# Optimization experiments

Measured on AMD Instinct MI355X. Metric: run time of the kernel, lower is better.

The kernel has to match this reference:

```python
import jax, jax.numpy as jnp
import numpy as np
from jax import lax

N = 5000
C = 81  # num_classes including background at index 0
BG_OFFSET = 1


def _iou_matrix(b):
    # b: [N,4] as x1,y1,x2,y2 -> pairwise IoU [N,N]
    x1, y1, x2, y2 = b[:, 0], b[:, 1], b[:, 2], b[:, 3]
    area = (x2 - x1) * (y2 - y1)  # [N]
    ix1 = jnp.maximum(x1[:, None], x1[None, :])
    iy1 = jnp.maximum(y1[:, None], y1[None, :])
    ix2 = jnp.minimum(x2[:, None], x2[None, :])
    iy2 = jnp.minimum(y2[:, None], y2[None, :])
    iw = jnp.maximum(ix2 - ix1, 0.0)
    ih = jnp.maximum(iy2 - iy1, 0.0)
    inter = iw * ih
    return inter / (area[:, None] + area[None, :] - inter)


def setup_inputs() -> dict:
    key = jax.random.key(0)
    k1, k2, k3 = jax.random.split(key, 3)
    # valid boxes: x1<x2, y1<y2 on a ~1024px canvas, size ~up to 256px
    xy1 = jax.random.uniform(k1, (N, 2), dtype=jnp.float32) * 1024.0
    wh = jax.random.uniform(k2, (N, 2), dtype=jnp.float32) * 256.0 + 1.0
    bboxes = jnp.concatenate([xy1, xy1 + wh], axis=1)  # [N,4]
    scores = jax.random.uniform(k3, (N, C), dtype=jnp.float32)  # [N,C]
    return {
        "bboxes": bboxes,
        "scores": scores,
        "conf_thresh": 0.6,
        "nms_thresh": 0.5,
        "max_instances": 300,
    }


def _multiclass_nms(bboxes, scores, conf_thresh, nms_thresh, max_instances):
    n = bboxes.shape[0]
    neg_inf = jnp.finfo(scores.dtype).min
    iou = _iou_matrix(bboxes)  # [N,N]

    def nms_one_class(score_c):  # score_c: [N]
        valid = score_c > conf_thresh
        masked = jnp.where(valid, score_c, neg_inf)
        order = jnp.argsort(masked)[::-1]  # descending score

        def step(suppressed, idx):
            keep = valid[idx] & ~suppressed[idx]
            new_sup = jnp.where(keep, suppressed | (iou[idx] > nms_thresh), suppressed)
            return new_sup, keep

        _, keeps = lax.scan(step, jnp.zeros((n,), bool), order)
        # scatter keep flags back to original box order
        return jnp.zeros((n,), bool).at[order].set(keeps)

    fg_scores = scores[:, BG_OFFSET:].T  # [C-1, N]
    keep = jax.vmap(nms_one_class)(fg_scores)  # [C-1, N]

    # global top-k over all (class, box) kept detections, sorted by score desc
    flat = jnp.where(keep, fg_scores, neg_inf).reshape(-1)  # [(C-1)*N]
    top_scores, top_idx = lax.top_k(flat, max_instances)
    cls = top_idx // n + BG_OFFSET  # [K]
    box = top_idx % n  # [K]
    valid_out = top_scores > neg_inf / 2

    sel_score = scores[box, cls]  # differentiable gather
    preds = jnp.concatenate([bboxes[box], sel_score[:, None]], axis=1)  # [K,5]
    preds = jnp.where(valid_out[:, None], preds, 0.0)
    labels = jnp.where(valid_out, cls, -1)
    return preds, labels


def reference(bboxes, scores, conf_thresh, nms_thresh, max_instances):
    return _multiclass_nms(bboxes, scores, conf_thresh, nms_thresh, max_instances)
```

## Files before the change

kernel.cpp:

```cpp
#include <hip/hip_runtime.h>

typedef unsigned long long u64;
typedef unsigned int u32;
typedef unsigned short u16;

#define MSORT 4096
#define TPB1  1024
#define TPBF  1024
#define BOXCAP 3648
#define KCAP  3072
#define RSLOT_W 10
#define KPC   300
#define SELCAP 1024
#define PREFR 64

#define WG_SCOPE  __HIP_MEMORY_SCOPE_WORKGROUP
#define DEV_SCOPE __HIP_MEMORY_SCOPE_AGENT

__device__ __forceinline__ float boxArea(float4 b) {
    return __fmul_rn(__fsub_rn(b.z, b.x), __fsub_rn(b.w, b.y));
}

template<bool GE>
__device__ __forceinline__ bool iou_gt(float4 a, float area_a, float4 b, float area_b, double B) {
    float ix1 = fmaxf(a.x, b.x), iy1 = fmaxf(a.y, b.y);
    float ix2 = fminf(a.z, b.z), iy2 = fminf(a.w, b.w);
    float iw  = fmaxf(__fsub_rn(ix2, ix1), 0.0f);
    float ih  = fmaxf(__fsub_rn(iy2, iy1), 0.0f);
    float inter = __fmul_rn(iw, ih);
    float uni   = __fsub_rn(__fadd_rn(area_a, area_b), inter);
    return GE ? ((double)inter >= B * (double)uni) : ((double)inter > B * (double)uni);
}

__device__ __forceinline__ int scoreBin(u32 bits) {
    int b = (int)(bits >> 12) - 0x3F000;
    return b < 0 ? 0 : (b > 2047 ? 2047 : b);
}

__device__ __forceinline__ void bstar_wave0(
    const u32* __restrict__ hist, int target, int tid,
    int* __restrict__ outBs, int* __restrict__ outTot)
{
    if (tid < 64) {
        int s = 0;
        #pragma unroll
        for (int b = 0; b < 32; b++)
            s += (int)hist[(tid << 5) + ((b + tid) & 31)];
        #pragma unroll
        for (int d = 1; d < 64; d <<= 1) {
            int v = __shfl_down(s, d, 64);
            if (tid + d < 64) s += v;
        }
        u64 bal = __ballot(s >= target);
        int ch  = bal ? (63 - __builtin_clzll(bal)) : -1;
        int tot = __shfl(s, 0, 64);
        int bs  = 0;
        if (ch >= 0) {
            int accAbove = (ch < 63) ? __shfl(s, ch + 1, 64) : 0;
            int h = (tid < 32) ? (int)hist[(ch << 5) + tid] : 0;
            #pragma unroll
            for (int d = 1; d < 32; d <<= 1) {
                int v = __shfl_down(h, d, 64);
                if (tid + d < 32) h += v;
            }
            u64 bal2 = __ballot((tid < 32) && (accAbove + h >= target));
            bs = (ch << 5) + (63 - __builtin_clzll(bal2));
        }
        if (tid == 0) { *outBs = bs; if (outTot) *outTot = tot; }
    }
}

template<bool GE>
__device__ __forceinline__ int prefix_nms_w0(
    const float* __restrict__ bboxes, const u64* __restrict__ sorted,
    int R, double B, int tid, int c, int N, u64* __restrict__ gkept_c,
    u32* __restrict__ gHist)
{
    u64 key = (tid < R) ? sorted[tid] : 0;
    float4 bx = make_float4(0.f, 0.f, 0.f, 0.f);
    if (tid < R) bx = ((const float4*)bboxes)[(u32)key];
    float ar = boxArea(bx);
    u64 supB = (R >= 64) ? 0ull : (~0ull << R);
    int nk = 0;
    int i = -1;
    for (;;) {
        u64 mask = (i >= 63) ? 0ull : (~0ull << (i + 1));
        u64 alive = ~supB & mask;
        if (!alive) break;
        i = (int)__builtin_ctzll(alive);
        float4 bi;
        bi.x = __shfl(bx.x, i, 64); bi.y = __shfl(bx.y, i, 64);
        bi.z = __shfl(bx.z, i, 64); bi.w = __shfl(bx.w, i, 64);
        float ai = boxArea(bi);
        if (tid == 0) {
            u64 ki = sorted[i];
            u32 flat = (u32)c * (u32)N + (u32)ki;
            gkept_c[nk] = (ki & 0xFFFFFFFF00000000ull) | (u32)(~flat);
        }
        nk++;
        bool sup = (tid > i) && iou_gt<GE>(bi, ai, bx, ar, B);
        supB |= __ballot(sup);
    }
    if (tid < R && !((supB >> tid) & 1ull))
        atomicAdd(&gHist[scoreBin((u32)(key >> 32))], 1u);
    return nk;
}

__global__ __launch_bounds__(TPB1, 1) void nms_select_kernel(
    const float* __restrict__ bboxes, const float* __restrict__ scores,
    const float* __restrict__ conf_ptr, const float* __restrict__ nms_ptr,
    int N, int C, u64* __restrict__ gkept,
    u32* __restrict__ gK, u32* __restrict__ g65, u32* __restrict__ gPre,
    u32* __restrict__ gHist, u32* __restrict__ gCtl, u32* __restrict__ gDone,
    int Mout)
{
    __shared__ u64 keys[KCAP];
    __shared__ u32 hist[2048];
    __shared__ u64 keybuf[256];
    __shared__ u64 sorted[66];
    __shared__ int cntS, ncollS, bstarS, nkS, lastS, thBs, thTot;

    const int tid = threadIdx.x;
    const int c   = blockIdx.x;
    const int cls = c + 1;
    const float conf = *conf_ptr;
    const float nmsT = *nms_ptr;

    for (int b = tid; b < 2048; b += TPB1) hist[b] = 0;
    if (tid < 66) sorted[tid] = 0;
    if (tid == 0) { cntS = 0; ncollS = 0; nkS = 0; }
    __syncthreads();

    for (int i = tid; i < N; i += TPB1) {
        float s = scores[(size_t)i * C + cls];
        if (s > conf) {
            int p = atomicAdd(&cntS, 1);
            if (p < KCAP) keys[p] = ((u64)__float_as_uint(s) << 32) | (u32)i;
            atomicAdd(&hist[scoreBin(__float_as_uint(s))], 1u);
        }
    }
    __syncthreads();
    const int K = cntS;
    const bool preOv = (K > KCAP);
    const int target = K < (PREFR + 1) ? K : (PREFR + 1);

    bstar_wave0(hist, target, tid, &bstarS, nullptr);
    __syncthreads();
    const u32 tbits = (bstarS == 0) ? 0u : (((u32)bstarS + 0x3F000u) << 12);

    const int KL = K < KCAP ? K : KCAP;
    for (int p = tid; p < KL; p += TPB1) {
        u64 k = keys[p];
        if ((u32)(k >> 32) >= tbits) {
            int pos = atomicAdd(&ncollS, 1);
            if (pos < 256) keybuf[pos] = k;
        }
    }
    __syncthreads();
    const int ncoll = ncollS;
    const bool pre = preOv || (ncoll > 256);
    for (int p = ncoll + tid; p < 256; p += TPB1) keybuf[p] = 0;
    __syncthreads();

    u64* gkept_c = gkept + (size_t)c * KPC;
    if (!pre) {
        if (tid < 256) {
            u64 my = keybuf[tid];
            int rank = 0;
            for (int j = 0; j < 256; j++) rank += (keybuf[j] > my);
            if (my && rank < PREFR + 1) sorted[rank] = my;
        }
        __syncthreads();
        const u32 tb = __float_as_uint(nmsT);
        const float Tn = __uint_as_float(tb + 1u);
        const double B = ((double)nmsT + (double)Tn) * 0.5;
        const bool geCmp = (((tb + 1u) & 1u) == 0u);
        if (tid < 64) {
            int R = ncoll < PREFR ? ncoll : PREFR;
            int nk = geCmp ? prefix_nms_w0<true >(bboxes, sorted, R, B, tid, c, N, gkept_c, gHist)
                           : prefix_nms_w0<false>(bboxes, sorted, R, B, tid, c, N, gkept_c, gHist);
            if (tid == 0) nkS = nk;
        }
        __syncthreads();
        for (int p = nkS + tid; p < KPC; p += TPB1) gkept_c[p] = 0;
    } else {
        for (int p = tid; p < KPC; p += TPB1) gkept_c[p] = 0;
    }
    if (tid == 0) {
        gK[c]   = (u32)K;
        g65[c]  = pre ? 0xFFFFFFFFu : ((ncoll >= PREFR + 1) ? (u32)(sorted[PREFR] >> 32) : 0u);
        gPre[c] = pre ? 1u : 0u;
    }

    __syncthreads();
    if (tid == 0)
        lastS = (__hip_atomic_fetch_add(gDone, 1u, __ATOMIC_ACQ_REL, DEV_SCOPE)
                 == (u32)(gridDim.x - 1)) ? 1 : 0;
    __syncthreads();
    if (!lastS) return;
    __threadfence();

    for (int b = tid; b < 2048; b += TPB1) hist[b] = gHist[b];
    __syncthreads();
    bstar_wave0(hist, Mout, tid, &thBs, &thTot);
    __syncthreads();
    u32 theta = 0u;
    if (thTot >= Mout && thBs > 0) theta = (((u32)thBs + 0x3F000u) << 12);
    if (tid == 0) gCtl[0] = theta;
    const int nclass = (int)gridDim.x;
    for (int c2 = tid; c2 < nclass; c2 += TPB1) {
        u32 need = gPre[c2];
        if (gK[c2] > PREFR && g65[c2] >= theta) need = 1u;
        gCtl[1 + c2] = need;
    }
}

template<bool GE>
__device__ __forceinline__ u64 sweep_own(
    float4 bi, float area_i, const float4 (&breg)[RSLOT_W],
    const float (&areaj)[RSLOT_W], const float4* __restrict__ boxesLds,
    int base, int nslots, int lane, double B)
{
    u64 ns = 0;
    #pragma unroll
    for (int t = 0; t < RSLOT_W; t++)
        ns |= ((u64)iou_gt<GE>(bi, area_i, breg[t], areaj[t], B)) << (base + t);
    for (int t = RSLOT_W; t < nslots; t++) {
        float4 bj = boxesLds[((base + t) << 6) | lane];
        ns |= ((u64)iou_gt<GE>(bi, area_i, bj, boxArea(bj), B)) << (base + t);
    }
    return ns;
}

template<bool GE>
__device__ __forceinline__ int greedy_full(
    const float4* __restrict__ boxesLds, u16* __restrict__ keptR,
    float4* __restrict__ pubBox, u32* __restrict__ ctl,
    const u32* __restrict__ gsi_c, const float* __restrict__ scores,
    int cls, int C, u32 thetaBits,
    int K, int smax, double B, int lane, int wave)
{
    const int SW   = (smax + 3) >> 2;
    const int base = (wave * SW < smax) ? wave * SW : smax;
    const int end  = (base + SW < smax) ? base + SW : smax;
    const int nslots = end - base;

    float4 breg[RSLOT_W];
    float  areaj[RSLOT_W];
    #pragma unroll
    for (int t = 0; t < RSLOT_W; t++) {
        float4 b = boxesLds[((base + t) << 6) | lane];
        breg[t] = b;
        areaj[t] = boxArea(b);
    }

    u64 sup;
    {
        int t = (lane < K) ? ((K - lane + 63) >> 6) : 0;
        sup = (t >= 64) ? 0ull : (~0ull << t);
    }

    u32 seen = 0;
    if (wave != 0) {
        for (;;) {
            u32 d  = __hip_atomic_load(&ctl[2], __ATOMIC_ACQUIRE, WG_SCOPE);
            u32 cn = __hip_atomic_load(&ctl[0], __ATOMIC_ACQUIRE, WG_SCOPE);
            bool prog = (seen < cn);
            while (seen < cn) {
                float4 bi = pubBox[seen]; seen++;
                sup |= sweep_own<GE>(bi, boxArea(bi), breg, areaj, boxesLds, base, nslots, lane, B);
            }
            if (d) return -1;
            u32 aw = __hip_atomic_load(&ctl[1], __ATOMIC_ACQUIRE, WG_SCOPE);
            if (aw == (u32)wave) {
                u32 cn2 = __hip_atomic_load(&ctl[0], __ATOMIC_ACQUIRE, WG_SCOPE);
                while (seen < cn2) {
                    float4 bi = pubBox[seen]; seen++;
                    sup |= sweep_own<GE>(bi, boxArea(bi), breg, areaj, boxesLds, base, nslots, lane, B);
                }
                break;
            }
            if (!prog) __builtin_amdgcn_s_sleep(1);
        }
    }

    u32 nk = seen;
    const u32 seen0 = seen;
    int scur = base - 1;
    float4 bcur = make_float4(0.f, 0.f, 0.f, 0.f);
    float  acur = 0.f;
    int js = base << 6;

    for (;;) {
        int s = js >> 6;
        while (s > scur) {
            scur++;
            if (scur < end) {
                bcur = boxesLds[(scur << 6) | lane];
                acur = boxArea(bcur);
                u64 bit = 0;
                for (u32 k = seen0; k < nk; k++) {
                    float4 bk = pubBox[k];
                    bit |= ((u64)iou_gt<GE>(bk, boxArea(bk), bcur, acur, B));
                }
                sup |= bit << scur;
            }
        }
        if (scur >= end) {
            if (wave == 3) {
                if (lane == 0) __hip_atomic_store(&ctl[2], 1u, __ATOMIC_RELEASE, WG_SCOPE);
                return (int)nk;
            }
            if (lane == 0) __hip_atomic_store(&ctl[1], (u32)(wave + 1), __ATOMIC_RELEASE, WG_SCOPE);
            return -1;
        }
        u64 bal = __ballot((int)(((~sup) >> scur) & 1ull)) & (~0ull << (js & 63));
        if (bal == 0) { js = (scur + 1) << 6; continue; }
        int i = (scur << 6) + (int)__builtin_ctzll(bal);

        if (thetaBits) {
            u32 idx = gsi_c[i];
            float sc = scores[(size_t)idx * C + cls];
            if (__float_as_uint(sc) < thetaBits) {
                if (lane == 0) __hip_atomic_store(&ctl[2], 1u, __ATOMIC_RELEASE, WG_SCOPE);
                return (int)nk;
            }
        }
        float4 bi = boxesLds[i];
        if (lane == 0) { pubBox[nk] = bi; keptR[nk] = (u16)i; }
        nk++;
        if (nk >= KPC) {
            if (lane == 0) {
                __hip_atomic_store(&ctl[0], nk, __ATOMIC_RELEASE, WG_SCOPE);
                __hip_atomic_store(&ctl[2], 1u, __ATOMIC_RELEASE, WG_SCOPE);
            }
            return (int)nk;
        }
        if (lane == 0) __hip_atomic_store(&ctl[0], nk, __ATOMIC_RELEASE, WG_SCOPE);
        sup |= ((u64)iou_gt<GE>(bi, boxArea(bi), bcur, acur, B)) << scur;
        js = i + 1;
    }
}

__global__ __launch_bounds__(TPBF, 1) void nms_full_topk_kernel(
    const float* __restrict__ bboxes, const float* __restrict__ scores,
    const float* __restrict__ conf_ptr, const float* __restrict__ nms_ptr,
    int N, int C, const u32* __restrict__ gCtl,
    u32* __restrict__ gsi, u64* __restrict__ gkept,
    int Mout, float* __restrict__ out, u32* __restrict__ gDone)
{
    __shared__ __align__(16) char smem[63856];
    __shared__ int cntS, lastS, selCountS, bs4S;

    const int c = blockIdx.x;
    const int tid = threadIdx.x;

    if (gCtl[1 + c] != 0u) {
        u64*    sortbuf  = (u64*)smem;
        float4* boxesLds = (float4*)smem;
        u16*    keptR    = (u16*)(smem + 58368);
        u32*    ctl      = (u32*)(smem + 58976);
        float4* pubBox   = (float4*)(smem + 58992);

        const int cls = c + 1;
        const float conf = *conf_ptr;
        const float nmsT = *nms_ptr;
        const u32 thetaBits = gCtl[0];

        if (tid == 0) cntS = 0;
        __syncthreads();
        for (int i = tid; i < N; i += TPBF) {
            float s = scores[(size_t)i * C + cls];
            if (s > conf) {
                int p = atomicAdd(&cntS, 1);
                if (p < MSORT) sortbuf[p] = ((u64)__float_as_uint(s) << 32) | (u32)i;
            }
        }
        __syncthreads();
        int K = cntS; if (K > BOXCAP) K = BOXCAP;
        int M = 64; while (M < K) M <<= 1;
        for (int p = K + tid; p < M; p += TPBF) sortbuf[p] = 0;
        __syncthreads();
        for (int kk = 2; kk <= M; kk <<= 1) {
            for (int j = kk >> 1; j > 0; j >>= 1) {
                for (int i = tid; i < M; i += TPBF) {
                    int ixj = i ^ j;
                    if (ixj > i) {
                        u64 a = sortbuf[i], b = sortbuf[ixj];
                        if (((i & kk) == 0) ? (a < b) : (a > b)) { sortbuf[i] = b; sortbuf[ixj] = a; }
                    }
                }
                __syncthreads();
            }
        }
        u32 myIdx[MSORT / TPBF];
        #pragma unroll
        for (int t = 0; t < MSORT / TPBF; t++) myIdx[t] = (u32)sortbuf[t * TPBF + tid];
        __syncthreads();
        u32* gsi_c = gsi + (size_t)c * BOXCAP;
        #pragma unroll
        for (int t = 0; t < MSORT / TPBF; t++) {
            int r = t * TPBF + tid;
            if (r < K) {
                u32 idx = myIdx[t];
                gsi_c[r] = idx;
                boxesLds[r] = ((const float4*)bboxes)[idx];
            }
        }
        if (tid == 0) { ctl[0] = 0; ctl[1] = 0; ctl[2] = 0; }
        __syncthreads();

        if (tid < 256) {
            const int lane = tid & 63;
            const int wave = tid >> 6;
            const u32 tb = __float_as_uint(nmsT);
            const float Tn = __uint_as_float(tb + 1u);
            const double B = ((double)nmsT + (double)Tn) * 0.5;
            const bool geCmp = (((tb + 1u) & 1u) == 0u);
            const int smax = (K + 63) >> 6;

            int ret = geCmp ? greedy_full<true >(boxesLds, keptR, pubBox, ctl, gsi_c, scores, cls, C, thetaBits, K, smax, B, lane, wave)
                            : greedy_full<false>(boxesLds, keptR, pubBox, ctl, gsi_c, scores, cls, C, thetaBits, K, smax, B, lane, wave);
            if (ret >= 0) {
                int kept = ret; if (kept > KPC) kept = KPC;
                u64* gkept_c = gkept + (size_t)c * KPC;
                for (int p = lane; p < kept; p += 64) {
                    int rank = keptR[p];
                    u32 idx = gsi_c[rank];
                    float sc = scores[(size_t)idx * C + cls];
                    u32 flat = (u32)c * (u32)N + idx;
                    gkept_c[p] = ((u64)__float_as_uint(sc) << 32) | (u32)(~flat);
                }
                for (int p = kept + lane; p < KPC; p += 64) gkept_c[p] = 0;
            }
        }
    }

    __syncthreads();
    if (tid == 0)
        lastS = (__hip_atomic_fetch_add(gDone, 1u, __ATOMIC_ACQ_REL, DEV_SCOPE)
                 == (u32)(gridDim.x - 1)) ? 1 : 0;
    __syncthreads();
    if (!lastS) return;
    __threadfence();

    u64* sel   = (u64*)smem;
    u32* hist4 = (u32*)(smem + 8192);
    const int total = (int)gridDim.x * KPC;

    for (int b = tid; b < 2048; b += TPBF) hist4[b] = 0;
    if (tid == 0) selCountS = 0;
    __syncthreads();

    for (int t = tid; t < total; t += TPBF) {
        u64 k = gkept[t];
        if (k) atomicAdd(&hist4[scoreBin((u32)(k >> 32))], 1u);
    }
    __syncthreads();

    bstar_wave0(hist4, Mout, tid, &bs4S, nullptr);
    __syncthreads();
    const int bstar = bs4S;

    for (int t = tid; t < total; t += TPBF) {
        u64 k = gkept[t];
        if (k && scoreBin((u32)(k >> 32)) >= bstar) {
            int p = atomicAdd(&selCountS, 1);
            if (p < SELCAP) sel[p] = k;
        }
    }
    __syncthreads();
    int cnt = selCountS; if (cnt > SELCAP) cnt = SELCAP;
    int SM = 512; while (SM < cnt) SM <<= 1;
    for (int p = cnt + tid; p < SM; p += TPBF) sel[p] = 0;
    __syncthreads();

    for (int kk = 2; kk <= SM; kk <<= 1) {
        for (int j = kk >> 1; j > 0; j >>= 1) {
            for (int i = tid; i < SM; i += TPBF) {
                int ixj = i ^ j;
                if (ixj > i) {
                    u64 a = sel[i], b = sel[ixj];
                    if (((i & kk) == 0) ? (a < b) : (a > b)) { sel[i] = b; sel[ixj] = a; }
                }
            }
            __syncthreads();
        }
    }

    for (int t = tid; t < Mout; t += TPBF) {
        u64 k = (t < SM) ? sel[t] : 0;
        float px1 = 0.f, py1 = 0.f, px2 = 0.f, py2 = 0.f, ps = 0.f, plab = -1.0f;
        if (k) {
            float s  = __uint_as_float((u32)(k >> 32));
            u32 flat = ~((u32)k);
            int cc   = (int)(flat / (u32)N);
            int box  = (int)(flat - (u32)cc * (u32)N);
            float4 bb = ((const float4*)bboxes)[box];
            px1 = bb.x; py1 = bb.y; px2 = bb.z; py2 = bb.w; ps = s;
            plab = (float)(cc + 1);
        }
        out[t * 5 + 0] = px1;
        out[t * 5 + 1] = py1;
        out[t * 5 + 2] = px2;
        out[t * 5 + 3] = py2;
        out[t * 5 + 4] = ps;
        out[Mout * 5 + t] = plab;
    }
}

extern "C" void kernel_launch(void* const* d_in, const int* in_sizes, int n_in,
                              void* d_out, int out_size, void* d_ws, size_t ws_size,
                              hipStream_t stream) {
    const float* bboxes = (const float*)d_in[0];
    const float* scores = (const float*)d_in[1];
    const float* conf   = (const float*)d_in[2];
    const float* nmsT   = (const float*)d_in[3];

    const int N    = in_sizes[0] / 4;
    const int C    = in_sizes[1] / N;
    const int nc   = C - 1;
    const int Mout = out_size / 6;

    char* wsb = (char*)d_ws;
    size_t off = 0;
    u32* gsi   = (u32*)(wsb + off); off += (size_t)nc * BOXCAP * sizeof(u32);
    u64* gkept = (u64*)(wsb + off); off += (size_t)nc * KPC * sizeof(u64);
    u32* gK    = (u32*)(wsb + off); off += (size_t)((nc + 1) & ~1) * sizeof(u32);
    u32* g65   = (u32*)(wsb + off); off += (size_t)((nc + 1) & ~1) * sizeof(u32);
    u32* gPre  = (u32*)(wsb + off); off += (size_t)((nc + 1) & ~1) * sizeof(u32);
    u32* gCtl  = (u32*)(wsb + off); off += (size_t)((1 + nc + 1) & ~1) * sizeof(u32);
    u32* gHist = (u32*)(wsb + off); off += 2048 * sizeof(u32);
    u32* gDone = (u32*)(wsb + off); off += 2 * sizeof(u32);

    hipMemsetAsync(gHist, 0, (2048 + 2) * sizeof(u32), stream);

    nms_select_kernel<<<nc, TPB1, 0, stream>>>(bboxes, scores, conf, nmsT, N, C,
                                               gkept, gK, g65, gPre, gHist, gCtl,
                                               gDone, Mout);
    nms_full_topk_kernel<<<nc, TPBF, 0, stream>>>(bboxes, scores, conf, nmsT, N, C,
                                                  gCtl, gsi, gkept, Mout,
                                                  (float*)d_out, gDone + 1);
}
```

Baseline: 134.4 us.

## Transpose scores upfront and split last-block reductions into separate kernels

Adds a tiled transpose kernel that writes scores in class-major order, so the per-class scans read contiguous float4 rows instead of strided columns. It also replaces per-element LDS atomics with wave-aggregated ballot atomics. The last-block-done atomic pattern is replaced by standalone theta and top-k kernels, which removes the memset and device-scope atomics. The cost is an extra pass over the score matrix and three more kernel launches.

```diff
diff --git a/kernel.cpp b/kernel.cpp
--- a/kernel.cpp
+++ b/kernel.cpp
@@ -13,9 +13,9 @@
 #define KPC   300
 #define SELCAP 1024
 #define PREFR 64
-
-#define WG_SCOPE  __HIP_MEMORY_SCOPE_WORKGROUP
-#define DEV_SCOPE __HIP_MEMORY_SCOPE_AGENT
+#define TBOX  128
+
+#define WG_SCOPE __HIP_MEMORY_SCOPE_WORKGROUP
 
 __device__ __forceinline__ float boxArea(float4 b) {
     return __fmul_rn(__fsub_rn(b.z, b.x), __fsub_rn(b.w, b.y));
@@ -68,6 +68,35 @@
         }
         if (tid == 0) { *outBs = bs; if (outTot) *outTot = tot; }
     }
+}
+
+__global__ __launch_bounds__(1024) void transpose_kernel(
+    const float* __restrict__ scores, int N, int C,
+    float* __restrict__ scoresT, u32* __restrict__ gHist)
+{
+    __shared__ float tile[TBOX * 81];
+    const int tid = threadIdx.x;
+    const int b0  = blockIdx.x * TBOX;
+    const int nb  = (N - b0 < TBOX) ? (N - b0) : TBOX;
+    const int tot = nb * C;
+    for (int e = tid; e < tot; e += 1024)
+        tile[e] = scores[(size_t)b0 * C + e];
+    __syncthreads();
+    if (nb == TBOX) {
+        const int wtot = C << 7;
+        for (int o = tid; o < wtot; o += 1024) {
+            int cls = o >> 7, j = o & (TBOX - 1);
+            scoresT[(size_t)cls * N + b0 + j] = tile[j * C + cls];
+        }
+    } else {
+        const int wtot = C * nb;
+        for (int o = tid; o < wtot; o += 1024) {
+            int cls = o / nb, j = o - cls * nb;
+            scoresT[(size_t)cls * N + b0 + j] = tile[j * C + cls];
+        }
+    }
+    if (blockIdx.x == 0)
+        for (int h = tid; h < 2048; h += 1024) gHist[h] = 0;
 }
 
 template<bool GE>
@@ -107,22 +136,22 @@
 }
 
 __global__ __launch_bounds__(TPB1, 1) void nms_select_kernel(
-    const float* __restrict__ bboxes, const float* __restrict__ scores,
+    const float* __restrict__ bboxes, const float* __restrict__ scoresT,
     const float* __restrict__ conf_ptr, const float* __restrict__ nms_ptr,
-    int N, int C, u64* __restrict__ gkept,
+    int N, u64* __restrict__ gkept,
     u32* __restrict__ gK, u32* __restrict__ g65, u32* __restrict__ gPre,
-    u32* __restrict__ gHist, u32* __restrict__ gCtl, u32* __restrict__ gDone,
-    int Mout)
+    u32* __restrict__ gHist)
 {
     __shared__ u64 keys[KCAP];
     __shared__ u32 hist[2048];
     __shared__ u64 keybuf[256];
     __shared__ u64 sorted[66];
-    __shared__ int cntS, ncollS, bstarS, nkS, lastS, thBs, thTot;
-
-    const int tid = threadIdx.x;
-    const int c   = blockIdx.x;
-    const int cls = c + 1;
+    __shared__ int cntS, ncollS, bstarS, nkS;
+
+    const int tid  = threadIdx.x;
+    const int lane = tid & 63;
+    const int c    = blockIdx.x;
+    const int cls  = c + 1;
     const float conf = *conf_ptr;
     const float nmsT = *nms_ptr;
 
@@ -131,8 +160,32 @@
     if (tid == 0) { cntS = 0; ncollS = 0; nkS = 0; }
     __syncthreads();
 
-    for (int i = tid; i < N; i += TPB1) {
-        float s = scores[(size_t)i * C + cls];
+    const float* rowT = scoresT + (size_t)cls * N;
+    const float4* rowT4 = (const float4*)rowT;
+    const int N4 = N >> 2;
+    for (int i4 = tid; i4 < N4; i4 += TPB1) {
+        float4 s4 = rowT4[i4];
+        #pragma unroll
+        for (int j = 0; j < 4; j++) {
+            float s = (j == 0) ? s4.x : (j == 1) ? s4.y : (j == 2) ? s4.z : s4.w;
+            bool pass = (s > conf);
+            u64 m = __ballot(pass);
+            if (m) {
+                int leader = (int)__builtin_ctzll(m);
+                int base = 0;
+                if (lane == leader) base = atomicAdd(&cntS, __popcll(m));
+                base = __shfl(base, leader, 64);
+                if (pass) {
+                    int p = base + (int)__popcll(m & ((1ull << lane) - 1ull));
+                    if (p < KCAP)
+                        keys[p] = ((u64)__float_as_uint(s) << 32) | (u32)((i4 << 2) + j);
+                    atomicAdd(&hist[scoreBin(__float_as_uint(s))], 1u);
+                }
+            }
+        }
+    }
+    for (int i = (N4 << 2) + tid; i < N; i += TPB1) {
+        float s = rowT[i];
         if (s > conf) {
             int p = atomicAdd(&cntS, 1);
             if (p < KCAP) keys[p] = ((u64)__float_as_uint(s) << 32) | (u32)i;
@@ -191,24 +244,24 @@
         g65[c]  = pre ? 0xFFFFFFFFu : ((ncoll >= PREFR + 1) ? (u32)(sorted[PREFR] >> 32) : 0u);
         gPre[c] = pre ? 1u : 0u;
     }
-
-    __syncthreads();
-    if (tid == 0)
-        lastS = (__hip_atomic_fetch_add(gDone, 1u, __ATOMIC_ACQ_REL, DEV_SCOPE)
-                 == (u32)(gridDim.x - 1)) ? 1 : 0;
-    __syncthreads();
-    if (!lastS) return;
-    __threadfence();
-
-    for (int b = tid; b < 2048; b += TPB1) hist[b] = gHist[b];
+}
+
+__global__ __launch_bounds__(1024) void nms_theta_kernel(
+    const u32* __restrict__ gHist, const u32* __restrict__ gK,
+    const u32* __restrict__ g65, const u32* __restrict__ gPre,
+    int nc, int Mout, u32* __restrict__ gCtl)
+{
+    __shared__ u32 hist[2048];
+    __shared__ int thBs, thTot;
+    const int tid = threadIdx.x;
+    for (int b = tid; b < 2048; b += 1024) hist[b] = gHist[b];
     __syncthreads();
     bstar_wave0(hist, Mout, tid, &thBs, &thTot);
     __syncthreads();
     u32 theta = 0u;
     if (thTot >= Mout && thBs > 0) theta = (((u32)thBs + 0x3F000u) << 12);
     if (tid == 0) gCtl[0] = theta;
-    const int nclass = (int)gridDim.x;
-    for (int c2 = tid; c2 < nclass; c2 += TPB1) {
+    for (int c2 = tid; c2 < nc; c2 += 1024) {
         u32 need = gPre[c2];
         if (gK[c2] > PREFR && g65[c2] >= theta) need = 1u;
         gCtl[1 + c2] = need;
@@ -236,8 +289,8 @@
 __device__ __forceinline__ int greedy_full(
     const float4* __restrict__ boxesLds, u16* __restrict__ keptR,
     float4* __restrict__ pubBox, u32* __restrict__ ctl,
-    const u32* __restrict__ gsi_c, const float* __restrict__ scores,
-    int cls, int C, u32 thetaBits,
+    const u32* __restrict__ gsi_c, const float* __restrict__ rowT,
+    u32 thetaBits,
     int K, int smax, double B, int lane, int wave)
 {
     const int SW   = (smax + 3) >> 2;
@@ -320,7 +373,7 @@
 
         if (thetaBits) {
             u32 idx = gsi_c[i];
-            float sc = scores[(size_t)idx * C + cls];
+            float sc = rowT[idx];
             if (__float_as_uint(sc) < thetaBits) {
                 if (lane == 0) __hip_atomic_store(&ctl[2], 1u, __ATOMIC_RELEASE, WG_SCOPE);
                 return (int)nk;
@@ -342,142 +395,162 @@
     }
 }
 
-__global__ __launch_bounds__(TPBF, 1) void nms_full_topk_kernel(
-    const float* __restrict__ bboxes, const float* __restrict__ scores,
+__global__ __launch_bounds__(TPBF, 1) void nms_full_kernel(
+    const float* __restrict__ bboxes, const float* __restrict__ scoresT,
     const float* __restrict__ conf_ptr, const float* __restrict__ nms_ptr,
-    int N, int C, const u32* __restrict__ gCtl,
-    u32* __restrict__ gsi, u64* __restrict__ gkept,
-    int Mout, float* __restrict__ out, u32* __restrict__ gDone)
-{
+    int N, const u32* __restrict__ gCtl,
+    u32* __restrict__ gsi, u64* __restrict__ gkept)
+{
+    const int c = blockIdx.x;
+    if (gCtl[1 + c] == 0u) return;
+
     __shared__ __align__(16) char smem[63856];
-    __shared__ int cntS, lastS, selCountS, bs4S;
-
-    const int c = blockIdx.x;
+    u64*    sortbuf  = (u64*)smem;
+    float4* boxesLds = (float4*)smem;
+    u16*    keptR    = (u16*)(smem + 58368);
+    u32*    ctl      = (u32*)(smem + 58976);
+    float4* pubBox   = (float4*)(smem + 58992);
+    __shared__ int cntS;
+
+    const int tid  = threadIdx.x;
+    const int lane = tid & 63;
+    const int cls = c + 1;
+    const float conf = *conf_ptr;
+    const float nmsT = *nms_ptr;
+    const u32 thetaBits = gCtl[0];
+
+    if (tid == 0) cntS = 0;
+    __syncthreads();
+    const float* rowT = scoresT + (size_t)cls * N;
+    const float4* rowT4 = (const float4*)rowT;
+    const int N4 = N >> 2;
+    for (int i4 = tid; i4 < N4; i4 += TPBF) {
+        float4 s4 = rowT4[i4];
+        #pragma unroll
+        for (int j = 0; j < 4; j++) {
+            float s = (j == 0) ? s4.x : (j == 1) ? s4.y : (j == 2) ? s4.z : s4.w;
+            bool pass = (s > conf);
+            u64 m = __ballot(pass);
+            if (m) {
+                int leader = (int)__builtin_ctzll(m);
+                int base = 0;
+                if (lane == leader) base = atomicAdd(&cntS, __popcll(m));
+                base = __shfl(base, leader, 64);
+                if (pass) {
+                    int p = base + (int)__popcll(m & ((1ull << lane) - 1ull));
+                    if (p < MSORT)
+                        sortbuf[p] = ((u64)__float_as_uint(s) << 32) | (u32)((i4 << 2) + j);
+                }
+            }
+        }
+    }
+    for (int i = (N4 << 2) + tid; i < N; i += TPBF) {
+        float s = rowT[i];
+        if (s > conf) {
+            int p = atomicAdd(&cntS, 1);
+            if (p < MSORT) sortbuf[p] = ((u64)__float_as_uint(s) << 32) | (u32)i;
+        }
+    }
+    __syncthreads();
+    int K = cntS; if (K > BOXCAP) K = BOXCAP;
+    int M = 64; while (M < K) M <<= 1;
+    for (int p = K + tid; p < M; p += TPBF) sortbuf[p] = 0;
+    __syncthreads();
+    for (int kk = 2; kk <= M; kk <<= 1) {
+        for (int j = kk >> 1; j > 0; j >>= 1) {
+            for (int i = tid; i < M; i += TPBF) {
+                int ixj = i ^ j;
+                if (ixj > i) {
+                    u64 a = sortbuf[i], b = sortbuf[ixj];
+                    if (((i & kk) == 0) ? (a < b) : (a > b)) { sortbuf[i] = b; sortbuf[ixj] = a; }
+                }
+            }
+            __syncthreads();
+        }
+    }
+    u32 myIdx[MSORT / TPBF];
+    #pragma unroll
+    for (int t = 0; t < MSORT / TPBF; t++) myIdx[t] = (u32)sortbuf[t * TPBF + tid];
+    __syncthreads();
+    u32* gsi_c = gsi + (size_t)c * BOXCAP;
+    #pragma unroll
+    for (int t = 0; t < MSORT / TPBF; t++) {
+        int r = t * TPBF + tid;
+        if (r < K) {
+            u32 idx = myIdx[t];
+            gsi_c[r] = idx;
+            boxesLds[r] = ((const float4*)bboxes)[idx];
+        }
+    }
+    if (tid == 0) { ctl[0] = 0; ctl[1] = 0; ctl[2] = 0; }
+    __syncthreads();
+    if (tid >= 256) return;
+
+    const int wave = tid >> 6;
+    const u32 tb = __float_as_uint(nmsT);
+    const float Tn = __uint_as_float(tb + 1u);
+    const double B = ((double)nmsT + (double)Tn) * 0.5;
+    const bool geCmp = (((tb + 1u) & 1u) == 0u);
+    const int smax = (K + 63) >> 6;
+
+    int ret = geCmp ? greedy_full<true >(boxesLds, keptR, pubBox, ctl, gsi_c, rowT, thetaBits, K, smax, B, lane, wave)
+                    : greedy_full<false>(boxesLds, keptR, pubBox, ctl, gsi_c, rowT, thetaBits, K, smax, B, lane, wave);
+    if (ret >= 0) {
+        int kept = ret; if (kept > KPC) kept = KPC;
+        u64* gkept_c = gkept + (size_t)c * KPC;
+        for (int p = lane; p < kept; p += 64) {
+            int rank = keptR[p];
+            u32 idx = gsi_c[rank];
+            float sc = rowT[idx];
+            u32 flat = (u32)c * (u32)N + idx;
+            gkept_c[p] = ((u64)__float_as_uint(sc) << 32) | (u32)(~flat);
+        }
+        for (int p = kept + lane; p < KPC; p += 64) gkept_c[p] = 0;
+    }
+}
+
+__global__ __launch_bounds__(1024) void nms_topk_kernel(
+    const float* __restrict__ bboxes, const u64* __restrict__ gkept,
+    int N, int nc, int Mout, float* __restrict__ out)
+{
+    __shared__ u32 hist[2048];
+    __shared__ int selCount;
+    __shared__ int bstarS;
+    __shared__ u64 sel[SELCAP];
+
     const int tid = threadIdx.x;
-
-    if (gCtl[1 + c] != 0u) {
-        u64*    sortbuf  = (u64*)smem;
-        float4* boxesLds = (float4*)smem;
-        u16*    keptR    = (u16*)(smem + 58368);
-        u32*    ctl      = (u32*)(smem + 58976);
-        float4* pubBox   = (float4*)(smem + 58992);
-
-        const int cls = c + 1;
-        const float conf = *conf_ptr;
-        const float nmsT = *nms_ptr;
-        const u32 thetaBits = gCtl[0];
-
-        if (tid == 0) cntS = 0;
-        __syncthreads();
-        for (int i = tid; i < N; i += TPBF) {
-            float s = scores[(size_t)i * C + cls];
-            if (s > conf) {
-                int p = atomicAdd(&cntS, 1);
-                if (p < MSORT) sortbuf[p] = ((u64)__float_as_uint(s) << 32) | (u32)i;
-            }
-        }
-        __syncthreads();
-        int K = cntS; if (K > BOXCAP) K = BOXCAP;
-        int M = 64; while (M < K) M <<= 1;
-        for (int p = K + tid; p < M; p += TPBF) sortbuf[p] = 0;
-        __syncthreads();
-        for (int kk = 2; kk <= M; kk <<= 1) {
-            for (int j = kk >> 1; j > 0; j >>= 1) {
-                for (int i = tid; i < M; i += TPBF) {
-                    int ixj = i ^ j;
-                    if (ixj > i) {
-                        u64 a = sortbuf[i], b = sortbuf[ixj];
-                        if (((i & kk) == 0) ? (a < b) : (a > b)) { sortbuf[i] = b; sortbuf[ixj] = a; }
-                    }
-                }
-                __syncthreads();
-            }
-        }
-        u32 myIdx[MSORT / TPBF];
-        #pragma unroll
-        for (int t = 0; t < MSORT / TPBF; t++) myIdx[t] = (u32)sortbuf[t * TPBF + tid];
-        __syncthreads();
-        u32* gsi_c = gsi + (size_t)c * BOXCAP;
-        #pragma unroll
-        for (int t = 0; t < MSORT / TPBF; t++) {
-            int r = t * TPBF + tid;
-            if (r < K) {
-                u32 idx = myIdx[t];
-                gsi_c[r] = idx;
-                boxesLds[r] = ((const float4*)bboxes)[idx];
-            }
-        }
-        if (tid == 0) { ctl[0] = 0; ctl[1] = 0; ctl[2] = 0; }
-        __syncthreads();
-
-        if (tid < 256) {
-            const int lane = tid & 63;
-            const int wave = tid >> 6;
-            const u32 tb = __float_as_uint(nmsT);
-            const float Tn = __uint_as_float(tb + 1u);
-            const double B = ((double)nmsT + (double)Tn) * 0.5;
-            const bool geCmp = (((tb + 1u) & 1u) == 0u);
-            const int smax = (K + 63) >> 6;
-
-            int ret = geCmp ? greedy_full<true >(boxesLds, keptR, pubBox, ctl, gsi_c, scores, cls, C, thetaBits, K, smax, B, lane, wave)
-                            : greedy_full<false>(boxesLds, keptR, pubBox, ctl, gsi_c, scores, cls, C, thetaBits, K, smax, B, lane, wave);
-            if (ret >= 0) {
-                int kept = ret; if (kept > KPC) kept = KPC;
-                u64* gkept_c = gkept + (size_t)c * KPC;
-                for (int p = lane; p < kept; p += 64) {
-                    int rank = keptR[p];
-                    u32 idx = gsi_c[rank];
-                    float sc = scores[(size_t)idx * C + cls];
-                    u32 flat = (u32)c * (u32)N + idx;
-                    gkept_c[p] = ((u64)__float_as_uint(sc) << 32) | (u32)(~flat);
-                }
-                for (int p = kept + lane; p < KPC; p += 64) gkept_c[p] = 0;
-            }
-        }
-    }
-
-    __syncthreads();
-    if (tid == 0)
-        lastS = (__hip_atomic_fetch_add(gDone, 1u, __ATOMIC_ACQ_REL, DEV_SCOPE)
-                 == (u32)(gridDim.x - 1)) ? 1 : 0;
-    __syncthreads();
-    if (!lastS) return;
-    __threadfence();
-
-    u64* sel   = (u64*)smem;
-    u32* hist4 = (u32*)(smem + 8192);
-    const int total = (int)gridDim.x * KPC;
-
-    for (int b = tid; b < 2048; b += TPBF) hist4[b] = 0;
-    if (tid == 0) selCountS = 0;
-    __syncthreads();
-
-    for (int t = tid; t < total; t += TPBF) {
+    const int total = nc * KPC;
+
+    for (int b = tid; b < 2048; b += 1024) hist[b] = 0;
+    if (tid == 0) selCount = 0;
+    __syncthreads();
+
+    for (int t = tid; t < total; t += 1024) {
         u64 k = gkept[t];
-        if (k) atomicAdd(&hist4[scoreBin((u32)(k >> 32))], 1u);
-    }
-    __syncthreads();
-
-    bstar_wave0(hist4, Mout, tid, &bs4S, nullptr);
-    __syncthreads();
-    const int bstar = bs4S;
-
-    for (int t = tid; t < total; t += TPBF) {
+        if (k) atomicAdd(&hist[scoreBin((u32)(k >> 32))], 1u);
+    }
+    __syncthreads();
+
+    bstar_wave0(hist, Mout, tid, &bstarS, nullptr);
+    __syncthreads();
+    const int bstar = bstarS;
+
+    for (int t = tid; t < total; t += 1024) {
         u64 k = gkept[t];
         if (k && scoreBin((u32)(k >> 32)) >= bstar) {
-            int p = atomicAdd(&selCountS, 1);
+            int p = atomicAdd(&selCount, 1);
             if (p < SELCAP) sel[p] = k;
         }
     }
     __syncthreads();
-    int cnt = selCountS; if (cnt > SELCAP) cnt = SELCAP;
+    int cnt = selCount; if (cnt > SELCAP) cnt = SELCAP;
     int SM = 512; while (SM < cnt) SM <<= 1;
-    for (int p = cnt + tid; p < SM; p += TPBF) sel[p] = 0;
+    for (int p = cnt + tid; p < SM; p += 1024) sel[p] = 0;
     __syncthreads();
 
     for (int kk = 2; kk <= SM; kk <<= 1) {
         for (int j = kk >> 1; j > 0; j >>= 1) {
-            for (int i = tid; i < SM; i += TPBF) {
+            for (int i = tid; i < SM; i += 1024) {
                 int ixj = i ^ j;
                 if (ixj > i) {
                     u64 a = sel[i], b = sel[ixj];
@@ -488,7 +561,7 @@
         }
     }
 
-    for (int t = tid; t < Mout; t += TPBF) {
+    for (int t = tid; t < Mout; t += 1024) {
         u64 k = (t < SM) ? sel[t] : 0;
         float px1 = 0.f, py1 = 0.f, px2 = 0.f, py2 = 0.f, ps = 0.f, plab = -1.0f;
         if (k) {
@@ -524,6 +597,7 @@
 
     char* wsb = (char*)d_ws;
     size_t off = 0;
+    float* scoresT = (float*)(wsb + off); off += ((size_t)C * N * sizeof(float) + 255) & ~(size_t)255;
     u32* gsi   = (u32*)(wsb + off); off += (size_t)nc * BOXCAP * sizeof(u32);
     u64* gkept = (u64*)(wsb + off); off += (size_t)nc * KPC * sizeof(u64);
     u32* gK    = (u32*)(wsb + off); off += (size_t)((nc + 1) & ~1) * sizeof(u32);
@@ -531,14 +605,12 @@
     u32* gPre  = (u32*)(wsb + off); off += (size_t)((nc + 1) & ~1) * sizeof(u32);
     u32* gCtl  = (u32*)(wsb + off); off += (size_t)((1 + nc + 1) & ~1) * sizeof(u32);
     u32* gHist = (u32*)(wsb + off); off += 2048 * sizeof(u32);
-    u32* gDone = (u32*)(wsb + off); off += 2 * sizeof(u32);
-
-    hipMemsetAsync(gHist, 0, (2048 + 2) * sizeof(u32), stream);
-
-    nms_select_kernel<<<nc, TPB1, 0, stream>>>(bboxes, scores, conf, nmsT, N, C,
-                                               gkept, gK, g65, gPre, gHist, gCtl,
-                                               gDone, Mout);
-    nms_full_topk_kernel<<<nc, TPBF, 0, stream>>>(bboxes, scores, conf, nmsT, N, C,
-                                                  gCtl, gsi, gkept, Mout,
-                                                  (float*)d_out, gDone + 1);
-}
+
+    const int ntile = (N + TBOX - 1) / TBOX;
+    transpose_kernel<<<ntile, 1024, 0, stream>>>(scores, N, C, scoresT, gHist);
+    nms_select_kernel<<<nc, TPB1, 0, stream>>>(bboxes, scoresT, conf, nmsT, N,
+                                               gkept, gK, g65, gPre, gHist);
+    nms_theta_kernel<<<1, 1024, 0, stream>>>(gHist, gK, g65, gPre, nc, Mout, gCtl);
+    nms_full_kernel<<<nc, TPBF, 0, stream>>>(bboxes, scoresT, conf, nmsT, N, gCtl, gsi, gkept);
+    nms_topk_kernel<<<1, 1024, 0, stream>>>(bboxes, gkept, N, nc, Mout, (float*)d_out);
+}
```

After: 124.6 us. 7.3% less time.
